# Kernel optimization log

Measured on AMD Instinct MI355X. Metric: run time of the kernel, lower is better.

## Reference

```python
import jax, jax.numpy as jnp
import numpy as np

N, M, T_STEPS = 32, 64, 20000  # t = T/dt = 200/0.01
DT = 0.01
SQRT_DT = DT ** 0.5


def setup_inputs() -> dict:
    key = jax.random.key(0)
    k1, k2 = jax.random.split(key)
    # theta ~ U(lower, upper) per the module's prior (4-param variant)
    lower = jnp.array([0.5, 0.1, 0.1, 0.0], dtype=jnp.float32)
    upper = jnp.array([1.5, 3.0, 0.6, 4.0], dtype=jnp.float32)
    theta = lower + (upper - lower) * jax.random.uniform(k1, (N, 4), dtype=jnp.float32)
    noise = jax.random.normal(k2, (N, M, T_STEPS), dtype=jnp.float32)
    return {"theta": theta, "noise": noise}


def reference(theta, noise):
    # Euler-Maruyama OU recurrence: x_{i+1} = x_i + gamma*(mu - x_i)*dt + sigma*sqrt(dt)*eps_i
    n, m, t = noise.shape
    gamma = theta[:, 0][:, None]  # [n,1] broadcasts over m
    mu = theta[:, 1][:, None]
    sigma = theta[:, 2][:, None]
    x0 = jnp.broadcast_to(theta[:, 3][:, None], (n, m))

    eps_t = jnp.moveaxis(noise, -1, 0)  # [t, n, m] for scan

    def step(x, eps):
        x_new = x + gamma * (mu - x) * DT + sigma * SQRT_DT * eps
        return x_new, x_new

    _, xs = jax.lax.scan(step, x0, eps_t)  # xs: [t, n, m] == x[:, :, 1:]
    return jnp.moveaxis(xs, 0, -1)  # [n, m, t]
```

## Files before the change

kernel.cpp:

```cpp
#include <hip/hip_runtime.h>


#define T_STEPS 20000
#define M_PATHS 64
#define CHUNK   8
#define NWAVES  4
#define BLOCK   (NWAVES * 64)
#define BTILE   (BLOCK * CHUNK)
#define NBT     ((T_STEPS + BTILE - 1) / BTILE)
#define DT      0.01f
#define SQRT_DT 0.1f

__global__ __launch_bounds__(BLOCK, 8) void ou_scan_kernel(
    const float* __restrict__ theta,
    const float* __restrict__ noise,
    float* __restrict__ out)
{
    __shared__ float sA[2][NWAVES], sB[2][NWAVES];

    const int tid   = threadIdx.x;
    const int wave  = tid >> 6;
    const int lane  = tid & 63;
    const int chain = blockIdx.x;
    const int n     = chain >> 6;

    const float gamma = theta[n * 4 + 0];
    const float mu    = theta[n * 4 + 1];
    const float sigma = theta[n * 4 + 2];
    float carry       = theta[n * 4 + 3];

    const float a    = 1.0f - gamma * DT;
    const float gmdt = gamma * mu * DT;
    const float ssd  = sigma * SQRT_DT;
    const float a2 = a * a;
    const float a4 = a2 * a2;
    const float a8 = a4 * a4;

    const float* __restrict__ np_ = noise + (size_t)chain * T_STEPS;
    float* __restrict__       op_ = out   + (size_t)chain * T_STEPS;

    float4 c0, c1;
    {
        const int e0 = tid * CHUNK;
        c0 = *(const float4*)(np_ + e0);
        c1 = *(const float4*)(np_ + e0 + 4);
    }

    for (int tb = 0; tb < NBT; ++tb) {
        float4 n0 = make_float4(0.f, 0.f, 0.f, 0.f);
        float4 n1 = make_float4(0.f, 0.f, 0.f, 0.f);
        const int ne0 = (tb + 1) * BTILE + tid * CHUNK;
        if (ne0 + CHUNK <= T_STEPS) {
            n0 = *(const float4*)(np_ + ne0);
            n1 = *(const float4*)(np_ + ne0 + 4);
        }

        const int  base = tb * BTILE + tid * CHUNK;
        const bool act  = (base + CHUNK <= T_STEPS);

        const float b0 = fmaf(ssd, c0.x, gmdt);
        const float b1 = fmaf(ssd, c0.y, gmdt);
        const float b2 = fmaf(ssd, c0.z, gmdt);
        const float b3 = fmaf(ssd, c0.w, gmdt);
        const float b4 = fmaf(ssd, c1.x, gmdt);
        const float b5 = fmaf(ssd, c1.y, gmdt);
        const float b6 = fmaf(ssd, c1.z, gmdt);
        const float b7 = fmaf(ssd, c1.w, gmdt);

        float p = b0;
        p = fmaf(p, a, b1);
        p = fmaf(p, a, b2);
        p = fmaf(p, a, b3);
        p = fmaf(p, a, b4);
        p = fmaf(p, a, b5);
        p = fmaf(p, a, b6);
        p = fmaf(p, a, b7);

        float A = act ? a8 : 1.0f;
        float B = act ? p  : 0.0f;

        #pragma unroll
        for (int d = 1; d < 64; d <<= 1) {
            const float pA = __shfl_up(A, d);
            const float pB = __shfl_up(B, d);
            if (lane >= d) {
                B = fmaf(A, pB, B);
                A = A * pA;
            }
        }

        if (lane == 63) { sA[tb & 1][wave] = A; sB[tb & 1][wave] = B; }
        __syncthreads();

        float PA = 1.f, PB = 0.f, FA = 1.f, FB = 0.f;
        #pragma unroll
        for (int w = 0; w < NWAVES; ++w) {
            const float aw = sA[tb & 1][w];
            const float bw = sB[tb & 1][w];
            if (w < wave) { PB = fmaf(aw, PB, bw); PA *= aw; }
            FB = fmaf(aw, FB, bw); FA *= aw;
        }

        const float xw = fmaf(PA, carry, PB);

        float Aex = __shfl_up(A, 1);
        float Bex = __shfl_up(B, 1);
        if (lane == 0) { Aex = 1.f; Bex = 0.f; }
        float x = fmaf(Aex, xw, Bex);

        carry = fmaf(FA, carry, FB);

        if (act) {
            float4 o0, o1;
            x = fmaf(a, x, b0); o0.x = x;
            x = fmaf(a, x, b1); o0.y = x;
            x = fmaf(a, x, b2); o0.z = x;
            x = fmaf(a, x, b3); o0.w = x;
            x = fmaf(a, x, b4); o1.x = x;
            x = fmaf(a, x, b5); o1.y = x;
            x = fmaf(a, x, b6); o1.z = x;
            x = fmaf(a, x, b7); o1.w = x;
            *(float4*)(op_ + base)     = o0;
            *(float4*)(op_ + base + 4) = o1;
        }

        c0 = n0;
        c1 = n1;
    }
}

extern "C" void kernel_launch(void* const* d_in, const int* in_sizes, int n_in,
                              void* d_out, int out_size, void* d_ws, size_t ws_size,
                              hipStream_t stream) {
    const float* theta = (const float*)d_in[0];
    const float* noise = (const float*)d_in[1];
    float* out = (float*)d_out;

    const int chains = in_sizes[1] / T_STEPS;
    ou_scan_kernel<<<chains, BLOCK, 0, stream>>>(theta, noise, out);
}
```

Before: 288.8 us.

## Precompute closed-form powers of decay to drop multiplier scan; double chunk size

The per-lane chunk grows from 8 to 16 steps. The multiplicative half of the affine scan is replaced by closed-form powers of the decay factor, since every active lane shares the same multiplier. This halves the shuffles and removes a shared-memory array. Bias terms are recomputed rather than kept live, and outputs use nontemporal vector stores. The trade-off is more registers per thread and fewer tiles to overlap load latency. It also relies on every active lane covering a full chunk.

```diff
diff --git a/kernel.cpp b/kernel.cpp
--- a/kernel.cpp
+++ b/kernel.cpp
@@ -3,7 +3,7 @@
 
 #define T_STEPS 20000
 #define M_PATHS 64
-#define CHUNK   8
+#define CHUNK   16
 #define NWAVES  4
 #define BLOCK   (NWAVES * 64)
 #define BTILE   (BLOCK * CHUNK)
@@ -11,12 +11,14 @@
 #define DT      0.01f
 #define SQRT_DT 0.1f
 
+typedef float f32x4 __attribute__((ext_vector_type(4)));
+
 __global__ __launch_bounds__(BLOCK, 8) void ou_scan_kernel(
     const float* __restrict__ theta,
     const float* __restrict__ noise,
     float* __restrict__ out)
 {
-    __shared__ float sA[2][NWAVES], sB[2][NWAVES];
+    __shared__ float sB[2][NWAVES];
 
     const int tid   = threadIdx.x;
     const int wave  = tid >> 6;
@@ -32,100 +34,132 @@
     const float a    = 1.0f - gamma * DT;
     const float gmdt = gamma * mu * DT;
     const float ssd  = sigma * SQRT_DT;
-    const float a2 = a * a;
-    const float a4 = a2 * a2;
-    const float a8 = a4 * a4;
+
+    const float a2    = a * a;
+    const float a4    = a2 * a2;
+    const float a8    = a4 * a4;
+    const float a16   = a8 * a8;
+    const float a32   = a16 * a16;
+    const float a64   = a32 * a32;
+    const float a128  = a64 * a64;
+    const float a256  = a128 * a128;
+    const float a512  = a256 * a256;
+    const float a1024 = a512 * a512;
+    const float a2048 = a1024 * a1024;
+    const float a4096 = a2048 * a2048;
+
+    float Aex = 1.f;
+    if (lane & 1)  Aex *= a16;
+    if (lane & 2)  Aex *= a32;
+    if (lane & 4)  Aex *= a64;
+    if (lane & 8)  Aex *= a128;
+    if (lane & 16) Aex *= a256;
+    if (lane & 32) Aex *= a512;
+
+    float PA = 1.f;
+    if (wave & 1) PA *= a1024;
+    if (wave & 2) PA *= a2048;
+    const float FA = a4096;
 
     const float* __restrict__ np_ = noise + (size_t)chain * T_STEPS;
     float* __restrict__       op_ = out   + (size_t)chain * T_STEPS;
 
-    float4 c0, c1;
+    float4 c0, c1, c2, c3;
     {
         const int e0 = tid * CHUNK;
         c0 = *(const float4*)(np_ + e0);
         c1 = *(const float4*)(np_ + e0 + 4);
+        c2 = *(const float4*)(np_ + e0 + 8);
+        c3 = *(const float4*)(np_ + e0 + 12);
     }
 
     for (int tb = 0; tb < NBT; ++tb) {
-        float4 n0 = make_float4(0.f, 0.f, 0.f, 0.f);
-        float4 n1 = make_float4(0.f, 0.f, 0.f, 0.f);
+        float4 n0 = make_float4(0.f,0.f,0.f,0.f), n1 = n0, n2 = n0, n3 = n0;
         const int ne0 = (tb + 1) * BTILE + tid * CHUNK;
         if (ne0 + CHUNK <= T_STEPS) {
             n0 = *(const float4*)(np_ + ne0);
             n1 = *(const float4*)(np_ + ne0 + 4);
+            n2 = *(const float4*)(np_ + ne0 + 8);
+            n3 = *(const float4*)(np_ + ne0 + 12);
         }
 
         const int  base = tb * BTILE + tid * CHUNK;
         const bool act  = (base + CHUNK <= T_STEPS);
 
-        const float b0 = fmaf(ssd, c0.x, gmdt);
-        const float b1 = fmaf(ssd, c0.y, gmdt);
-        const float b2 = fmaf(ssd, c0.z, gmdt);
-        const float b3 = fmaf(ssd, c0.w, gmdt);
-        const float b4 = fmaf(ssd, c1.x, gmdt);
-        const float b5 = fmaf(ssd, c1.y, gmdt);
-        const float b6 = fmaf(ssd, c1.z, gmdt);
-        const float b7 = fmaf(ssd, c1.w, gmdt);
+        float p;
+        p = fmaf(ssd, c0.x, gmdt);
+        p = fmaf(p, a, fmaf(ssd, c0.y, gmdt));
+        p = fmaf(p, a, fmaf(ssd, c0.z, gmdt));
+        p = fmaf(p, a, fmaf(ssd, c0.w, gmdt));
+        p = fmaf(p, a, fmaf(ssd, c1.x, gmdt));
+        p = fmaf(p, a, fmaf(ssd, c1.y, gmdt));
+        p = fmaf(p, a, fmaf(ssd, c1.z, gmdt));
+        p = fmaf(p, a, fmaf(ssd, c1.w, gmdt));
+        p = fmaf(p, a, fmaf(ssd, c2.x, gmdt));
+        p = fmaf(p, a, fmaf(ssd, c2.y, gmdt));
+        p = fmaf(p, a, fmaf(ssd, c2.z, gmdt));
+        p = fmaf(p, a, fmaf(ssd, c2.w, gmdt));
+        p = fmaf(p, a, fmaf(ssd, c3.x, gmdt));
+        p = fmaf(p, a, fmaf(ssd, c3.y, gmdt));
+        p = fmaf(p, a, fmaf(ssd, c3.z, gmdt));
+        p = fmaf(p, a, fmaf(ssd, c3.w, gmdt));
 
-        float p = b0;
-        p = fmaf(p, a, b1);
-        p = fmaf(p, a, b2);
-        p = fmaf(p, a, b3);
-        p = fmaf(p, a, b4);
-        p = fmaf(p, a, b5);
-        p = fmaf(p, a, b6);
-        p = fmaf(p, a, b7);
+        float B = act ? p : 0.f;
 
-        float A = act ? a8 : 1.0f;
-        float B = act ? p  : 0.0f;
-
-        #pragma unroll
-        for (int d = 1; d < 64; d <<= 1) {
-            const float pA = __shfl_up(A, d);
-            const float pB = __shfl_up(B, d);
-            if (lane >= d) {
-                B = fmaf(A, pB, B);
-                A = A * pA;
-            }
+        {
+            float t;
+            t = __shfl_up(B, 1);  if (lane >= 1)  B = fmaf(a16,  t, B);
+            t = __shfl_up(B, 2);  if (lane >= 2)  B = fmaf(a32,  t, B);
+            t = __shfl_up(B, 4);  if (lane >= 4)  B = fmaf(a64,  t, B);
+            t = __shfl_up(B, 8);  if (lane >= 8)  B = fmaf(a128, t, B);
+            t = __shfl_up(B, 16); if (lane >= 16) B = fmaf(a256, t, B);
+            t = __shfl_up(B, 32); if (lane >= 32) B = fmaf(a512, t, B);
         }
 
-        if (lane == 63) { sA[tb & 1][wave] = A; sB[tb & 1][wave] = B; }
+        if (lane == 63) sB[tb & 1][wave] = B;
         __syncthreads();
 
-        float PA = 1.f, PB = 0.f, FA = 1.f, FB = 0.f;
+        float PB = 0.f, pb = 0.f;
         #pragma unroll
-        for (int w = 0; w < NWAVES; ++w) {
-            const float aw = sA[tb & 1][w];
-            const float bw = sB[tb & 1][w];
-            if (w < wave) { PB = fmaf(aw, PB, bw); PA *= aw; }
-            FB = fmaf(aw, FB, bw); FA *= aw;
+        for (int v = 0; v < NWAVES; ++v) {
+            if (v == wave) PB = pb;
+            pb = fmaf(pb, a1024, sB[tb & 1][v]);
         }
+        const float FB = pb;
 
         const float xw = fmaf(PA, carry, PB);
 
-        float Aex = __shfl_up(A, 1);
         float Bex = __shfl_up(B, 1);
-        if (lane == 0) { Aex = 1.f; Bex = 0.f; }
+        if (lane == 0) Bex = 0.f;
         float x = fmaf(Aex, xw, Bex);
 
         carry = fmaf(FA, carry, FB);
 
         if (act) {
-            float4 o0, o1;
-            x = fmaf(a, x, b0); o0.x = x;
-            x = fmaf(a, x, b1); o0.y = x;
-            x = fmaf(a, x, b2); o0.z = x;
-            x = fmaf(a, x, b3); o0.w = x;
-            x = fmaf(a, x, b4); o1.x = x;
-            x = fmaf(a, x, b5); o1.y = x;
-            x = fmaf(a, x, b6); o1.z = x;
-            x = fmaf(a, x, b7); o1.w = x;
-            *(float4*)(op_ + base)     = o0;
-            *(float4*)(op_ + base + 4) = o1;
+            f32x4 o0, o1, o2, o3;
+            x = fmaf(a, x, fmaf(ssd, c0.x, gmdt)); o0.x = x;
+            x = fmaf(a, x, fmaf(ssd, c0.y, gmdt)); o0.y = x;
+            x = fmaf(a, x, fmaf(ssd, c0.z, gmdt)); o0.z = x;
+            x = fmaf(a, x, fmaf(ssd, c0.w, gmdt)); o0.w = x;
+            x = fmaf(a, x, fmaf(ssd, c1.x, gmdt)); o1.x = x;
+            x = fmaf(a, x, fmaf(ssd, c1.y, gmdt)); o1.y = x;
+            x = fmaf(a, x, fmaf(ssd, c1.z, gmdt)); o1.z = x;
+            x = fmaf(a, x, fmaf(ssd, c1.w, gmdt)); o1.w = x;
+            x = fmaf(a, x, fmaf(ssd, c2.x, gmdt)); o2.x = x;
+            x = fmaf(a, x, fmaf(ssd, c2.y, gmdt)); o2.y = x;
+            x = fmaf(a, x, fmaf(ssd, c2.z, gmdt)); o2.z = x;
+            x = fmaf(a, x, fmaf(ssd, c2.w, gmdt)); o2.w = x;
+            x = fmaf(a, x, fmaf(ssd, c3.x, gmdt)); o3.x = x;
+            x = fmaf(a, x, fmaf(ssd, c3.y, gmdt)); o3.y = x;
+            x = fmaf(a, x, fmaf(ssd, c3.z, gmdt)); o3.z = x;
+            x = fmaf(a, x, fmaf(ssd, c3.w, gmdt)); o3.w = x;
+            __builtin_nontemporal_store(o0, (f32x4*)(op_ + base));
+            __builtin_nontemporal_store(o1, (f32x4*)(op_ + base + 4));
+            __builtin_nontemporal_store(o2, (f32x4*)(op_ + base + 8));
+            __builtin_nontemporal_store(o3, (f32x4*)(op_ + base + 12));
         }
 
-        c0 = n0;
-        c1 = n1;
+        c0 = n0; c1 = n1; c2 = n2; c3 = n3;
     }
 }
 
```

Measured after the change: 366.9 us. +27.1%, slower.
